# Performance work log

Measured on AMD Instinct MI355X. Metric: run time of the kernel, lower is better.

## Reference

```python
import jax, jax.numpy as jnp
import numpy as np

N_S, N_T, E = 50000, 50000, 600000
D_IN, D_H, D_OUT = 256, 128, 64


def setup_inputs() -> dict:
    key = jax.random.key(0)
    k1, k2, k3, k4, k5, k6 = jax.random.split(key, 6)
    edge_src = jax.random.randint(k1, (E,), 0, N_S, dtype=jnp.int32)
    edge_dst = jax.random.randint(k2, (E,), 0, N_T, dtype=jnp.int32)
    edge_index = jnp.stack([edge_src, edge_dst], axis=0)  # [2, E]
    x_s = jax.random.normal(k3, (N_S, D_IN), dtype=jnp.float32)
    x_t = jax.random.normal(k4, (N_T, D_IN), dtype=jnp.float32)
    W0 = jax.random.normal(k5, (D_IN, D_H), dtype=jnp.float32) * (1.0 / np.sqrt(D_IN))
    W1 = jax.random.normal(k6, (D_H, D_OUT), dtype=jnp.float32) * (1.0 / np.sqrt(D_H))
    return {"edge_index": edge_index, "x_s": x_s, "x_t": x_t, "W0": W0, "W1": W1}


def gcn_conv(x, src, dst, W):
    """PyG GCNConv, bias=False: D^{-1/2}(A+I)D^{-1/2} (x @ W)."""
    N = x.shape[0]
    h = x @ W  # [N, out]
    loops = jnp.arange(N, dtype=src.dtype)
    s = jnp.concatenate([src, loops])  # add self-loops
    d = jnp.concatenate([dst, loops])
    deg = jax.ops.segment_sum(jnp.ones_like(d, dtype=h.dtype), d, num_segments=N)
    dinv = jnp.where(deg > 0, jax.lax.rsqrt(deg), 0.0)
    norm = dinv[s] * dinv[d]  # [E+N]
    return jax.ops.segment_sum(h[s] * norm[:, None], d, num_segments=N)


def reference(edge_index, x_s, x_t, W0, W1):
    n_s = x_s.shape[0]
    src = edge_index[0]
    dst = edge_index[1] + n_s  # targets live in the x_t block
    acts = [jax.nn.relu, lambda v: v]
    Ws = [W0, W1]
    for W, act in zip(Ws, acts):
        x = jnp.concatenate([x_s, x_t], axis=0)
        x = act(gcn_conv(x, src, dst, W))
        x_s, x_t = x[:n_s], x[n_s:]
    return (x_s, x_t)
```

## Files before the change

### kernel.cpp

```cpp
#include <hip/hip_runtime.h>
#include <cstdint>
#include <cstddef>

typedef unsigned short u16;
typedef unsigned int   u32;
typedef __attribute__((ext_vector_type(8))) short bf16x8;
typedef __attribute__((ext_vector_type(4))) float f32x4;

#define D_IN  256
#define D_H   128
#define D_OUT 64

__device__ __forceinline__ float bf2f(u16 u){
  union { u32 i; float f; } v; v.i = ((u32)u) << 16; return v.f;
}
__device__ __forceinline__ u16 f2bf(float f){
  union { float f; u32 i; } v; v.f = f;
  u32 r = (v.i + 0x7fffu + ((v.i >> 16) & 1u)) >> 16;
  return (u16)r;
}

__global__ void k_wprep(const float* __restrict__ W0, const float* __restrict__ W1,
                        u16* __restrict__ W0t, u16* __restrict__ W1t,
                        int* __restrict__ deg, int n_t){
  int i = blockIdx.x * 256 + threadIdx.x;
  if (i < 128 * 256){
    int n = i >> 8, k = i & 255;
    W0t[i] = f2bf(W0[(size_t)k * 128 + n]);
  } else if (i < 128 * 256 + 64 * 128){
    int j = i - 128 * 256;
    int n = j >> 7, k = j & 127;
    W1t[j] = f2bf(W1[(size_t)k * 64 + n]);
  } else if (i - (128 * 256 + 64 * 128) < n_t){
    deg[i - (128 * 256 + 64 * 128)] = 0;
  }
}

__global__ __launch_bounds__(256) void k_off(const int* __restrict__ deg, int N,
                                             int* __restrict__ off, int* __restrict__ cursor,
                                             float* __restrict__ dinv){
  __shared__ int s[256];
  __shared__ int sbase[256];
  const int tid = threadIdx.x;
  const int bid = blockIdx.x;
  const int i   = bid * 256 + tid;
  int acc = 0;
  const int lim = bid * 256;
  for (int j = tid; j < lim; j += 256) acc += deg[j];
  sbase[tid] = acc;
  int v = (i < N) ? deg[i] : 0;
  s[tid] = v;
  __syncthreads();
  for (int o = 128; o > 0; o >>= 1){
    if (tid < o) sbase[tid] += sbase[tid + o];
    __syncthreads();
  }
  for (int o = 1; o < 256; o <<= 1){
    int tv = (tid >= o) ? s[tid - o] : 0;
    __syncthreads();
    s[tid] += tv;
    __syncthreads();
  }
  if (i < N){
    int excl = s[tid] - v + sbase[0];
    off[i] = excl;
    cursor[i] = excl;
    dinv[i] = rsqrtf((float)v + 1.0f);
  }
}

__global__ void k_fill(const int* __restrict__ src, const int* __restrict__ dst,
                       int E, int* __restrict__ cursor, int* __restrict__ csr){
  int e = blockIdx.x * 256 + threadIdx.x;
  if (e < E){
    int d = dst[e];
    int p = atomicAdd(&cursor[d], 1);
    csr[p] = src[e];
  }
}

__global__ __launch_bounds__(512, 4) void k_g1deg(
    const float* __restrict__ Xs, const float* __restrict__ Xt,
    const u16* __restrict__ W0t, int M, int n_s,
    const int* __restrict__ dst, int E, int* __restrict__ deg,
    u16* __restrict__ out)
{
  __shared__ u16 Bs[128 * 256];
  const int t    = threadIdx.x;
  const int wave = t >> 6, lane = t & 63;
  const int lm   = lane & 15, quad = lane >> 4;
  const int gw   = blockIdx.x * 8 + wave;
  const int row  = gw * 16 + lm;

  int cr = (row < M) ? row : 0;
  const float* pa = ((cr < n_s) ? (Xs + (size_t)cr * D_IN)
                                : (Xt + (size_t)(cr - n_s) * D_IN)) + quad * 8;

  float4 a[8][2];
  a[0][0] = *(const float4*)(pa +  0); a[0][1] = *(const float4*)(pa +  4);
  a[1][0] = *(const float4*)(pa + 32); a[1][1] = *(const float4*)(pa + 36);

  {
    const int stride = (int)gridDim.x * 512;
    int e = blockIdx.x * 512 + t;
    if (e < E) atomicAdd(&deg[dst[e]], 1);
    e += stride;
    if (e < E) atomicAdd(&deg[dst[e]], 1);
    for (e += stride; e < E; e += stride) atomicAdd(&deg[dst[e]], 1);
  }

  {
    const int n = t >> 2;
    const int c = t & 3;
    const u16* wsrc = W0t + (size_t)n * 256 + c * 64;
    char* brow = (char*)Bs + n * 512;
    const int sw = (n & 15) << 4;
    #pragma unroll
    for (int j = 0; j < 8; j++){
      int off = (c * 128 + j * 16) ^ sw;
      *(int4*)(brow + off) = *(const int4*)(wsrc + j * 8);
    }
  }

  #pragma unroll
  for (int s = 2; s < 8; s++){
    a[s][0] = *(const float4*)(pa + s * 32);
    a[s][1] = *(const float4*)(pa + s * 32 + 4);
  }
  __builtin_amdgcn_sched_barrier(0);

  f32x4 acc[8];
  const f32x4 z = {0.f, 0.f, 0.f, 0.f};
  #pragma unroll
  for (int nf = 0; nf < 8; nf++) acc[nf] = z;

  __syncthreads();

  const char* bb = (const char*)Bs + lm * 512;
  const int lmx = lm << 4;

  #pragma unroll
  for (int kk = 0; kk < 8; kk++){
    bf16x8 af;
    {
      const float* fa = (const float*)&a[kk][0];
      u16 tmp[8];
      #pragma unroll
      for (int q = 0; q < 8; q++) tmp[q] = f2bf(fa[q]);
      af = *(const bf16x8*)tmp;
    }
    const int koff = (kk * 64 + quad * 16) ^ lmx;
    #pragma unroll
    for (int nf = 0; nf < 8; nf++){
      bf16x8 bf = *(const bf16x8*)(bb + nf * 8192 + koff);
      acc[nf] = __builtin_amdgcn_mfma_f32_16x16x32_bf16(af, bf, acc[nf], 0, 0, 0);
    }
  }

  {
    int rbase = gw * 16 + quad * 4;
    #pragma unroll
    for (int rr = 0; rr < 4; rr++){
      int m = rbase + rr;
      if (m >= M) continue;
      u16* op = out + (size_t)m * D_H + lm;
      #pragma unroll
      for (int nf = 0; nf < 8; nf++)
        op[nf * 16] = f2bf(acc[nf][rr]);
    }
  }
}

__device__ __forceinline__ void aggf_body(
    const int* __restrict__ off, const int* __restrict__ deg,
    const int* __restrict__ csr, const float* __restrict__ dinv,
    u16* __restrict__ h1, int n_s, int n_t, int w, int lane)
{
  if (w >= n_t) return;
  const int g = lane >> 4;
  const int c = lane & 15;
  int start = off[w];
  int n     = deg[w];

  float r[8], p[8];
  #pragma unroll
  for (int q = 0; q < 8; q++){ r[q] = 0.f; p[q] = 0.f; }

  int i = 0;
  for (; i + 8 <= n; i += 8){
    int sa = csr[start + i + g];
    int sb = csr[start + i + 4 + g];
    int4 da = *(const int4*)(h1 + (size_t)sa * D_H + c * 8);
    int4 db = *(const int4*)(h1 + (size_t)sb * D_H + c * 8);
    const u16* ha = (const u16*)&da;
    const u16* hb = (const u16*)&db;
    #pragma unroll
    for (int q = 0; q < 8; q++){
      float va = bf2f(ha[q]), vb = bf2f(hb[q]);
      r[q] += va + vb;
      p[q] += fmaxf(va, 0.f) + fmaxf(vb, 0.f);
    }
  }
  for (; i < n; i += 4){
    if (i + g < n){
      int sa = csr[start + i + g];
      int4 da = *(const int4*)(h1 + (size_t)sa * D_H + c * 8);
      const u16* ha = (const u16*)&da;
      #pragma unroll
      for (int q = 0; q < 8; q++){
        float va = bf2f(ha[q]);
        r[q] += va;
        p[q] += fmaxf(va, 0.f);
      }
    }
  }

  #pragma unroll
  for (int q = 0; q < 8; q++){
    r[q] += __shfl_xor(r[q], 16, 64);
    r[q] += __shfl_xor(r[q], 32, 64);
    p[q] += __shfl_xor(p[q], 16, 64);
    p[q] += __shfl_xor(p[q], 32, 64);
  }

  if (g == 0){
    float di  = dinv[w];
    float di2 = di * di;
    u16* selfp = h1 + (size_t)(n_s + w) * D_H + c * 8;
    int4 hs = *(const int4*)selfp;
    const u16* hh = (const u16*)&hs;
    u16 ob[8];
    #pragma unroll
    for (int q = 0; q < 8; q++){
      float zq = fmaxf(di * r[q] + di2 * bf2f(hh[q]), 0.f);
      float uq = di * p[q] + di2 * zq;
      ob[q] = f2bf(uq);
    }
    *(int4*)selfp = *(int4*)ob;
  }
}

__device__ __forceinline__ bf16x8 relu_bf(int4 v, bool relu){
  const u16* s = (const u16*)&v;
  u16 tmp[8];
  #pragma unroll
  for (int q = 0; q < 8; q++){
    u16 x = s[q];
    tmp[q] = (relu && (x & 0x8000u)) ? (u16)0 : x;
  }
  return *(const bf16x8*)tmp;
}

__device__ __forceinline__ void gemm2_body(
    const u16* __restrict__ h1, const u16* __restrict__ W1t,
    int gb, int base, int rowLim, int n_s, float* __restrict__ out,
    u16* Bs)
{
  const int t    = threadIdx.x;
  const int wave = t >> 6, lane = t & 63;
  const int lm   = lane & 15, quad = lane >> 4;
  const int gw   = gb * 8 + wave;
  const int row  = base + gw * 16 + lm;

  int cr = (row < rowLim) ? row : base;
  const bool relu = (cr < n_s);
  const u16* pa = h1 + (size_t)cr * D_H + quad * 8;

  int4 a[4];
  a[0] = *(const int4*)(pa);
  a[1] = *(const int4*)(pa + 32);

  {
    const int n = t >> 3;
    const int c = t & 7;
    const u16* wsrc = W1t + (size_t)n * 128 + c * 16;
    char* brow = (char*)Bs + n * 256;
    const int sw = (n & 15) << 4;
    #pragma unroll
    for (int j = 0; j < 2; j++){
      int off = (c * 32 + j * 16) ^ sw;
      *(int4*)(brow + off) = *(const int4*)(wsrc + j * 8);
    }
  }
  a[2] = *(const int4*)(pa + 64);
  a[3] = *(const int4*)(pa + 96);
  __builtin_amdgcn_sched_barrier(0);

  f32x4 acc[4];
  const f32x4 z = {0.f, 0.f, 0.f, 0.f};
  #pragma unroll
  for (int nf = 0; nf < 4; nf++) acc[nf] = z;

  __syncthreads();

  const char* bb = (const char*)Bs + lm * 256;
  const int lmx = lm << 4;

  #pragma unroll
  for (int kk = 0; kk < 4; kk++){
    bf16x8 af = relu_bf(a[kk], relu);
    const int koff = (kk * 64 + quad * 16) ^ lmx;
    #pragma unroll
    for (int nf = 0; nf < 4; nf++){
      bf16x8 bf = *(const bf16x8*)(bb + nf * 4096 + koff);
      acc[nf] = __builtin_amdgcn_mfma_f32_16x16x32_bf16(af, bf, acc[nf], 0, 0, 0);
    }
  }

  {
    int rbase = base + gw * 16 + quad * 4;
    #pragma unroll
    for (int rr = 0; rr < 4; rr++){
      int m = rbase + rr;
      if (m >= rowLim) continue;
      float* op = out + (size_t)m * D_OUT + lm;
      #pragma unroll
      for (int nf = 0; nf < 4; nf++)
        op[nf * 16] = acc[nf][rr];
    }
  }
}

__global__ __launch_bounds__(512, 4) void k_agg2s(
    const int* __restrict__ off, const int* __restrict__ deg,
    const int* __restrict__ csr, const float* __restrict__ dinv,
    u16* __restrict__ h1, int n_s, int n_t,
    const u16* __restrict__ W1t, float* __restrict__ out, int nbAgg)
{
  __shared__ u16 Bs[64 * 128];
  if ((int)blockIdx.x < nbAgg){
    int w = blockIdx.x * 8 + (threadIdx.x >> 6);
    aggf_body(off, deg, csr, dinv, h1, n_s, n_t, w, threadIdx.x & 63);
  } else {
    gemm2_body(h1, W1t, (int)blockIdx.x - nbAgg, 0, n_s, n_s, out, Bs);
  }
}

__global__ __launch_bounds__(512, 4) void k_g2t(
    const u16* __restrict__ h1, const u16* __restrict__ W1t,
    int M, int n_s, float* __restrict__ out)
{
  __shared__ u16 Bs[64 * 128];
  gemm2_body(h1, W1t, (int)blockIdx.x, n_s, M, n_s, out, Bs);
}

static inline size_t alup(size_t x){ return (x + 255) & ~(size_t)255; }

extern "C" void kernel_launch(void* const* d_in, const int* in_sizes, int n_in,
                              void* d_out, int out_size, void* d_ws, size_t ws_size,
                              hipStream_t stream)
{
  const int*   ei = (const int*)d_in[0];
  const float* xs = (const float*)d_in[1];
  const float* xt = (const float*)d_in[2];
  const float* W0 = (const float*)d_in[3];
  const float* W1 = (const float*)d_in[4];
  const int E   = in_sizes[0] / 2;
  const int n_s = in_sizes[1] / D_IN;
  const int n_t = in_sizes[2] / D_IN;
  const int M   = n_s + n_t;
  const int* src = ei;
  const int* dst = ei + E;

  char* p = (char*)d_ws;
  int*   deg    = (int*)p;    p += alup((size_t)n_t * 4);
  int*   off    = (int*)p;    p += alup((size_t)n_t * 4);
  int*   cursor = (int*)p;    p += alup((size_t)n_t * 4);
  float* dinv   = (float*)p;  p += alup((size_t)n_t * 4);
  int*   csr    = (int*)p;    p += alup((size_t)E * 4);
  u16*   W0t    = (u16*)p;    p += alup((size_t)D_H * D_IN * 2);
  u16*   W1t    = (u16*)p;    p += alup((size_t)D_OUT * D_H * 2);
  u16*   h1     = (u16*)p;    p += alup((size_t)M * D_H * 2);

  const int nb_t   = (n_t + 255) / 256;
  const int nbG1   = (M + 127) / 128;
  const int nbAgg  = (n_t + 7) / 8;
  const int nbG2s  = (n_s + 127) / 128;
  const int nbG2t  = (n_t + 127) / 128;

  const int wprep_n = 128*256 + 64*128 + n_t;
  k_wprep <<<(wprep_n + 255) / 256, 256, 0, stream>>>(W0, W1, W0t, W1t, deg, n_t);
  k_g1deg <<<nbG1, 512, 0, stream>>>(xs, xt, W0t, M, n_s, dst, E, deg, h1);
  k_off   <<<nb_t, 256, 0, stream>>>(deg, n_t, off, cursor, dinv);
  k_fill  <<<(E + 255) / 256, 256, 0, stream>>>(src, dst, E, cursor, csr);
  k_agg2s <<<nbAgg + nbG2s, 512, 0, stream>>>(off, deg, csr, dinv, h1, n_s, n_t,
                                              W1t, (float*)d_out, nbAgg);
  k_g2t   <<<nbG2t, 512, 0, stream>>>(h1, W1t, M, n_s, (float*)d_out);
}
```

Before: 270.1 us.

## Stage GEMM outputs through LDS for coalesced stores; split degree count into dedicated blocks

Both GEMM kernels now write their MFMA accumulators into a swizzled shared-memory tile and read them back as full 16-byte row vectors, so global stores are coalesced rows instead of scattered 2- or 4-byte writes. The degree-counting atomics move out of every GEMM1 block into 64 dedicated blocks at the front of the grid, so GEMM blocks no longer stall on atomics. The cost is extra LDS traffic and a barrier in GEMM1, plus an extra 32KB of shared memory per block in the GEMM2 kernels, which may lower occupancy there.

```diff
diff --git a/kernel.cpp b/kernel.cpp
--- a/kernel.cpp
+++ b/kernel.cpp
@@ -79,17 +79,25 @@
   }
 }
 
-__global__ __launch_bounds__(512, 4) void k_g1deg(
+__global__ __launch_bounds__(512, 4) void k_g1(
     const float* __restrict__ Xs, const float* __restrict__ Xt,
     const u16* __restrict__ W0t, int M, int n_s,
-    const int* __restrict__ dst, int E, int* __restrict__ deg,
+    const int* __restrict__ dst, int E, int* __restrict__ deg, int nbDeg,
     u16* __restrict__ out)
 {
   __shared__ u16 Bs[128 * 256];
-  const int t    = threadIdx.x;
+  const int t = threadIdx.x;
+
+  if ((int)blockIdx.x < nbDeg){
+    const int stride = nbDeg * 512;
+    for (int e = blockIdx.x * 512 + t; e < E; e += stride)
+      atomicAdd(&deg[dst[e]], 1);
+    return;
+  }
+
   const int wave = t >> 6, lane = t & 63;
   const int lm   = lane & 15, quad = lane >> 4;
-  const int gw   = blockIdx.x * 8 + wave;
+  const int gw   = ((int)blockIdx.x - nbDeg) * 8 + wave;
   const int row  = gw * 16 + lm;
 
   int cr = (row < M) ? row : 0;
@@ -99,15 +107,6 @@
   float4 a[8][2];
   a[0][0] = *(const float4*)(pa +  0); a[0][1] = *(const float4*)(pa +  4);
   a[1][0] = *(const float4*)(pa + 32); a[1][1] = *(const float4*)(pa + 36);
-
-  {
-    const int stride = (int)gridDim.x * 512;
-    int e = blockIdx.x * 512 + t;
-    if (e < E) atomicAdd(&deg[dst[e]], 1);
-    e += stride;
-    if (e < E) atomicAdd(&deg[dst[e]], 1);
-    for (e += stride; e < E; e += stride) atomicAdd(&deg[dst[e]], 1);
-  }
 
   {
     const int n = t >> 2;
@@ -157,16 +156,26 @@
     }
   }
 
+  __syncthreads();
+  u16* wreg = Bs + wave * 2048;
+  #pragma unroll
+  for (int nf = 0; nf < 8; nf++){
+    #pragma unroll
+    for (int rr = 0; rr < 4; rr++){
+      int rl = quad * 4 + rr;
+      int c  = nf * 16 + lm;
+      wreg[rl * 128 + (c ^ (quad << 5))] = f2bf(acc[nf][rr]);
+    }
+  }
   {
-    int rbase = gw * 16 + quad * 4;
-    #pragma unroll
-    for (int rr = 0; rr < 4; rr++){
-      int m = rbase + rr;
-      if (m >= M) continue;
-      u16* op = out + (size_t)m * D_H + lm;
-      #pragma unroll
-      for (int nf = 0; nf < 8; nf++)
-        op[nf * 16] = f2bf(acc[nf][rr]);
+    const int g = lane >> 4, l = lane & 15;
+    const int wrow0 = gw * 16;
+    #pragma unroll
+    for (int i = 0; i < 4; i++){
+      int rl = i * 4 + g;
+      int m  = wrow0 + rl;
+      bf16x8 v = *(const bf16x8*)&wreg[rl * 128 + ((l ^ (i << 2)) << 3)];
+      if (m < M) *(bf16x8*)(out + (size_t)m * D_H + l * 8) = v;
     }
   }
 }
@@ -254,7 +263,7 @@
 __device__ __forceinline__ void gemm2_body(
     const u16* __restrict__ h1, const u16* __restrict__ W1t,
     int gb, int base, int rowLim, int n_s, float* __restrict__ out,
-    u16* Bs)
+    u16* Bs, float* Cb)
 {
   const int t    = threadIdx.x;
   const int wave = t >> 6, lane = t & 63;
@@ -307,16 +316,25 @@
     }
   }
 
+  float* wreg = Cb + wave * 1024;
+  #pragma unroll
+  for (int nf = 0; nf < 4; nf++){
+    #pragma unroll
+    for (int rr = 0; rr < 4; rr++){
+      int rl = quad * 4 + rr;
+      int c  = nf * 16 + lm;
+      wreg[rl * 64 + (c ^ (quad << 4))] = acc[nf][rr];
+    }
+  }
   {
-    int rbase = base + gw * 16 + quad * 4;
-    #pragma unroll
-    for (int rr = 0; rr < 4; rr++){
-      int m = rbase + rr;
-      if (m >= rowLim) continue;
-      float* op = out + (size_t)m * D_OUT + lm;
-      #pragma unroll
-      for (int nf = 0; nf < 4; nf++)
-        op[nf * 16] = acc[nf][rr];
+    const int g = lane >> 4, l = lane & 15;
+    const int wrow0 = base + gw * 16;
+    #pragma unroll
+    for (int i = 0; i < 4; i++){
+      int rl = i * 4 + g;
+      int m  = wrow0 + rl;
+      float4 v = *(const float4*)&wreg[rl * 64 + ((l ^ (i << 2)) << 2)];
+      if (m < rowLim) *(float4*)(out + (size_t)m * D_OUT + l * 4) = v;
     }
   }
 }
@@ -327,12 +345,13 @@
     u16* __restrict__ h1, int n_s, int n_t,
     const u16* __restrict__ W1t, float* __restrict__ out, int nbAgg)
 {
-  __shared__ u16 Bs[64 * 128];
+  __shared__ u16  Bs[64 * 128];
+  __shared__ float Cb[8 * 1024];
   if ((int)blockIdx.x < nbAgg){
     int w = blockIdx.x * 8 + (threadIdx.x >> 6);
     aggf_body(off, deg, csr, dinv, h1, n_s, n_t, w, threadIdx.x & 63);
   } else {
-    gemm2_body(h1, W1t, (int)blockIdx.x - nbAgg, 0, n_s, n_s, out, Bs);
+    gemm2_body(h1, W1t, (int)blockIdx.x - nbAgg, 0, n_s, n_s, out, Bs, Cb);
   }
 }
 
@@ -340,8 +359,9 @@
     const u16* __restrict__ h1, const u16* __restrict__ W1t,
     int M, int n_s, float* __restrict__ out)
 {
-  __shared__ u16 Bs[64 * 128];
-  gemm2_body(h1, W1t, (int)blockIdx.x, n_s, M, n_s, out, Bs);
+  __shared__ u16  Bs[64 * 128];
+  __shared__ float Cb[8 * 1024];
+  gemm2_body(h1, W1t, (int)blockIdx.x, n_s, M, n_s, out, Bs, Cb);
 }
 
 static inline size_t alup(size_t x){ return (x + 255) & ~(size_t)255; }
@@ -373,6 +393,7 @@
   u16*   h1     = (u16*)p;    p += alup((size_t)M * D_H * 2);
 
   const int nb_t   = (n_t + 255) / 256;
+  const int nbDeg  = 64;
   const int nbG1   = (M + 127) / 128;
   const int nbAgg  = (n_t + 7) / 8;
   const int nbG2s  = (n_s + 127) / 128;
@@ -380,7 +401,7 @@
 
   const int wprep_n = 128*256 + 64*128 + n_t;
   k_wprep <<<(wprep_n + 255) / 256, 256, 0, stream>>>(W0, W1, W0t, W1t, deg, n_t);
-  k_g1deg <<<nbG1, 512, 0, stream>>>(xs, xt, W0t, M, n_s, dst, E, deg, h1);
+  k_g1    <<<nbDeg + nbG1, 512, 0, stream>>>(xs, xt, W0t, M, n_s, dst, E, deg, nbDeg, h1);
   k_off   <<<nb_t, 256, 0, stream>>>(deg, n_t, off, cursor, dinv);
   k_fill  <<<(E + 255) / 256, 256, 0, stream>>>(src, dst, E, cursor, csr);
   k_agg2s <<<nbAgg + nbG2s, 512, 0, stream>>>(off, deg, csr, dinv, h1, n_s, n_t,
```

Measured after the change: 259.9 us. 1.04x faster.
